# Kernel optimization log

Measured on AMD Instinct MI355X. Metric: run time of the kernel, lower is better.

## Reference

```python
import jax, jax.numpy as jnp
import numpy as np

B, A, D, K = 262144, 10, 10, 32  # batch, aspects, aspect dim (=10), projection dim


def setup_inputs() -> dict:
    key = jax.random.key(0)
    ks = jax.random.split(key, 7)
    scale = 0.01
    return {
        "user_rep": jax.random.normal(ks[0], (B, A, D), jnp.float32),
        "item_rep": jax.random.normal(ks[1], (B, A, D), jnp.float32),
        "affinity_matrix": jax.random.uniform(ks[2], (D, D), jnp.float32, -scale, scale),
        "user_projection": jax.random.uniform(ks[3], (K, D), jnp.float32, -scale, scale),
        "user_parameters": jax.random.uniform(ks[4], (K, 1), jnp.float32, -scale, scale),
        "item_projection": jax.random.uniform(ks[5], (K, D), jnp.float32, -scale, scale),
        "item_parameters": jax.random.uniform(ks[6], (K, 1), jnp.float32, -scale, scale),
    }


def reference(user_rep, item_rep, affinity_matrix, user_projection,
              user_parameters, item_projection, item_parameters):
    # affinity: relu( U @ M @ V^T )  -> [B, Au, Av]
    aff = jax.nn.relu(jnp.einsum('bud,de,bve->buv', user_rep, affinity_matrix, item_rep))

    h_user = jnp.einsum('kd,bud->bku', user_projection, user_rep)  # [B,K,Au]
    h_item = jnp.einsum('kd,bvd->bkv', item_projection, item_rep)  # [B,K,Av]

    # user importance branch
    hu = jax.nn.relu(h_user + jnp.einsum('bkv,buv->bku', h_item, aff))
    u_score = jnp.einsum('k,bku->bu', user_parameters[:, 0], hu)   # [B,Au]
    user_asp_importance = jax.nn.softmax(u_score, axis=1)

    # item importance branch
    hi = jax.nn.relu(h_item + jnp.einsum('bku,buv->bkv', h_user, aff))
    i_score = jnp.einsum('k,bkv->bv', item_parameters[:, 0], hi)   # [B,Av]
    item_asp_importance = jax.nn.softmax(i_score, axis=1)

    return (user_asp_importance, item_asp_importance)
```

## Files before the change

kernel.cpp:

```cpp
#include <hip/hip_runtime.h>

#define NB 262144
#define AA 10
#define DD 10
#define KK 32

typedef float v2f __attribute__((ext_vector_type(2)));

static __device__ __forceinline__ v2f mk2(float a, float b) {
    v2f r; r.x = a; r.y = b; return r;
}
static __device__ __forceinline__ v2f pk_fma(v2f a, v2f b, v2f c) {
    v2f d; asm("v_pk_fma_f32 %0, %1, %2, %3" : "=v"(d) : "v"(a), "v"(b), "v"(c)); return d;
}
static __device__ __forceinline__ v2f pk_fma_s(v2f sa, v2f b, v2f c) {
    v2f d; asm("v_pk_fma_f32 %0, %1, %2, %3" : "=v"(d) : "s"(sa), "v"(b), "v"(c)); return d;
}
static __device__ __forceinline__ v2f pk_mul(v2f a, v2f b) {
    v2f d; asm("v_pk_mul_f32 %0, %1, %2" : "=v"(d) : "v"(a), "v"(b)); return d;
}
static __device__ __forceinline__ v2f pk_mul_s(v2f sa, v2f b) {
    v2f d; asm("v_pk_mul_f32 %0, %1, %2" : "=v"(d) : "s"(sa), "v"(b)); return d;
}
static __device__ __forceinline__ v2f pk_add(v2f a, v2f b) {
    v2f d; asm("v_pk_add_f32 %0, %1, %2" : "=v"(d) : "v"(a), "v"(b)); return d;
}

static __device__ __forceinline__ float b2f(unsigned short h) {
    union { unsigned u; float f; } c; c.u = ((unsigned)h) << 16; return c.f;
}
static __device__ __forceinline__ float bflo(unsigned w) {
    union { unsigned u; float f; } c; c.u = w << 16; return c.f;
}
static __device__ __forceinline__ float bfhi(unsigned w) {
    union { unsigned u; float f; } c; c.u = w & 0xffff0000u; return c.f;
}

__device__ __forceinline__ int detect_f32(const unsigned short* p, int nshorts,
                                          unsigned expthr, int lane) {
    int bad = 0;
    if (lane < nshorts) {
        unsigned e = (p[lane] >> 7) & 0xFFu;
        bad = (e >= expthr);
    }
    return __any(bad);
}

__global__ __launch_bounds__(64) void prep_weights(
    const unsigned short* __restrict__ wM,
    const unsigned short* __restrict__ wPu,
    const unsigned short* __restrict__ wpu,
    const unsigned short* __restrict__ wPi,
    const unsigned short* __restrict__ wpi,
    float* __restrict__ wf)
{
    const int t = threadIdx.x;
    int f = 0;
    f |= detect_f32(wM,  64, 125, t) << 0;
    f |= detect_f32(wPu, 64, 125, t) << 1;
    f |= detect_f32(wpu, 32, 125, t) << 2;
    f |= detect_f32(wPi, 64, 125, t) << 3;
    f |= detect_f32(wpi, 32, 125, t) << 4;
    const float* fM  = (const float*)wM;
    const float* fPu = (const float*)wPu;
    const float* fpu = (const float*)wpu;
    const float* fPi = (const float*)wPi;
    const float* fpi = (const float*)wpi;

    for (int i = t; i < 100; i += 64) wf[i] = (f & 1) ? fM[i] : b2f(wM[i]);

    for (int i = t; i < KK * 24; i += 64) {
        const int k = i / 24, j = i % 24;
        float vu = 0.f, vi = 0.f;
        if (j < 10) {
            vu = (f & 2) ? fPu[k * 10 + j] : b2f(wPu[k * 10 + j]);
            vi = (f & 8) ? fPi[k * 10 + j] : b2f(wPi[k * 10 + j]);
        } else if (j < 20) {
            vu = (f & 8) ? fPi[k * 10 + j - 10] : b2f(wPi[k * 10 + j - 10]);
            vi = (f & 2) ? fPu[k * 10 + j - 10] : b2f(wPu[k * 10 + j - 10]);
        } else if (j == 20) {
            vu = (f & 4)  ? fpu[k] : b2f(wpu[k]);
            vi = (f & 16) ? fpi[k] : b2f(wpi[k]);
        }
        wf[128 + i] = vu;
        wf[896 + i] = vi;
    }
}

static __device__ __forceinline__ void load_rep(const unsigned short* __restrict__ p,
                                                int isf32, long long b, v2f R[AA][5]) {
    if (isf32) {
        const float4* g = (const float4*)((const float*)p + b * 100);
        #pragma unroll
        for (int j = 0; j < 25; j++) {
            float4 w = g[j];
            int e = 2 * j;
            R[e / 5][e % 5]             = mk2(w.x, w.y);
            R[(e + 1) / 5][(e + 1) % 5] = mk2(w.z, w.w);
        }
    } else {
        const uint2* g = (const uint2*)(p + b * 100);
        #pragma unroll
        for (int j = 0; j < 25; j++) {
            uint2 w = g[j];
            int e = 2 * j;
            R[e / 5][e % 5]             = mk2(bflo(w.x), bfhi(w.x));
            R[(e + 1) / 5][(e + 1) % 5] = mk2(bflo(w.y), bfhi(w.y));
        }
    }
}

__global__ __launch_bounds__(64, 2) void aie_main(
    const unsigned short* __restrict__ user_rep,
    const unsigned short* __restrict__ item_rep,
    const float* __restrict__ wf,
    float* __restrict__ out)
{
    __shared__ v2f stash[64 * 51];
    const int t = threadIdx.x;
    const long long b = (long long)blockIdx.x * 64 + t;
    v2f* my = &stash[t * 51];

    const int fu = detect_f32(user_rep, 64, 137, t);
    const int fi = detect_f32(item_rep, 64, 137, t);

    v2f U2[AA][5], V2[AA][5];
    load_rep(item_rep, fi, b, V2);
    load_rep(user_rep, fu, b, U2);

    const v2f* M2 = (const v2f*)wf;

    #pragma unroll
    for (int u = 0; u < AA; u++) {
        v2f um2[5];
        {
            v2f xs = mk2(U2[u][0].x, U2[u][0].x);
            #pragma unroll
            for (int j = 0; j < 5; j++) um2[j] = pk_mul_s(M2[j], xs);
        }
        #pragma unroll
        for (int d = 1; d < DD; d++) {
            const float x = (d & 1) ? U2[u][d >> 1].y : U2[u][d >> 1].x;
            v2f xs = mk2(x, x);
            #pragma unroll
            for (int j = 0; j < 5; j++) um2[j] = pk_fma_s(M2[d * 5 + j], xs, um2[j]);
        }
        v2f Wr[5];
        #pragma unroll
        for (int j = 0; j < 5; j++) Wr[j] = mk2(0.f, 0.f);
        #pragma unroll
        for (int v = 0; v < AA; v++) {
            v2f r2 = pk_mul(um2[0], V2[v][0]);
            #pragma unroll
            for (int j = 1; j < 5; j++) r2 = pk_fma(um2[j], V2[v][j], r2);
            const float r = fmaxf(r2.x + r2.y, 0.f);
            v2f rs = mk2(r, r);
            #pragma unroll
            for (int j = 0; j < 5; j++) Wr[j] = pk_fma(rs, V2[v][j], Wr[j]);
        }
        #pragma unroll
        for (int j = 0; j < 5; j++) my[u * 5 + j] = Wr[j];
    }
    asm volatile("" ::: "memory");

    v2f Wf[AA][5];
    #pragma unroll
    for (int u = 0; u < AA; u++)
        #pragma unroll
        for (int j = 0; j < 5; j++) Wf[u][j] = my[u * 5 + j];

    float us[AA];
    #pragma unroll
    for (int u = 0; u < AA; u++) us[u] = 0.f;
    #pragma unroll 2
    for (int k = 0; k < KK; k++) {
        const v2f* wk = (const v2f*)(wf + 128 + k * 24);
        const float pw = wf[128 + k * 24 + 20];
        #pragma unroll
        for (int u = 0; u < AA; u++) {
            v2f a2 = pk_mul_s(wk[0], U2[u][0]);
            v2f c2 = pk_mul_s(wk[5], Wf[u][0]);
            #pragma unroll
            for (int j = 1; j < 5; j++) {
                a2 = pk_fma_s(wk[j],     U2[u][j], a2);
                c2 = pk_fma_s(wk[5 + j], Wf[u][j], c2);
            }
            v2f s2 = pk_add(a2, c2);
            us[u] += pw * fmaxf(s2.x + s2.y, 0.f);
        }
    }

    {
        float mx = us[0];
        #pragma unroll
        for (int u = 1; u < AA; u++) mx = fmaxf(mx, us[u]);
        float s = 0.f;
        #pragma unroll
        for (int u = 0; u < AA; u++) { us[u] = __expf(us[u] - mx); s += us[u]; }
        const float inv = 1.f / s;
        float* o0 = out + b * 10;
        #pragma unroll
        for (int j = 0; j < 5; j++)
            *(float2*)(o0 + 2 * j) = make_float2(us[2 * j] * inv, us[2 * j + 1] * inv);
    }

    load_rep(item_rep, fi, b, V2);

    #pragma unroll
    for (int v = 0; v < AA; v++) {
        v2f mv2[5];
        #pragma unroll
        for (int dp = 0; dp < 5; dp++) {
            v2f s0 = pk_mul_s(M2[(2 * dp) * 5],     V2[v][0]);
            v2f s1 = pk_mul_s(M2[(2 * dp + 1) * 5], V2[v][0]);
            #pragma unroll
            for (int j = 1; j < 5; j++) {
                s0 = pk_fma_s(M2[(2 * dp) * 5 + j],     V2[v][j], s0);
                s1 = pk_fma_s(M2[(2 * dp + 1) * 5 + j], V2[v][j], s1);
            }
            mv2[dp] = mk2(s0.x + s0.y, s1.x + s1.y);
        }
        v2f Xr[5];
        #pragma unroll
        for (int j = 0; j < 5; j++) Xr[j] = mk2(0.f, 0.f);
        #pragma unroll
        for (int u = 0; u < AA; u++) {
            v2f r2 = pk_mul(mv2[0], U2[u][0]);
            #pragma unroll
            for (int j = 1; j < 5; j++) r2 = pk_fma(mv2[j], U2[u][j], r2);
            const float r = fmaxf(r2.x + r2.y, 0.f);
            v2f rs = mk2(r, r);
            #pragma unroll
            for (int j = 0; j < 5; j++) Xr[j] = pk_fma(rs, U2[u][j], Xr[j]);
        }
        #pragma unroll
        for (int j = 0; j < 5; j++) my[v * 5 + j] = Xr[j];
    }
    asm volatile("" ::: "memory");

    v2f Xf[AA][5];
    #pragma unroll
    for (int v = 0; v < AA; v++)
        #pragma unroll
        for (int j = 0; j < 5; j++) Xf[v][j] = my[v * 5 + j];

    float isc[AA];
    #pragma unroll
    for (int v = 0; v < AA; v++) isc[v] = 0.f;
    #pragma unroll 2
    for (int k = 0; k < KK; k++) {
        const v2f* wk = (const v2f*)(wf + 896 + k * 24);
        const float pw = wf[896 + k * 24 + 20];
        #pragma unroll
        for (int v = 0; v < AA; v++) {
            v2f a2 = pk_mul_s(wk[0], V2[v][0]);
            v2f c2 = pk_mul_s(wk[5], Xf[v][0]);
            #pragma unroll
            for (int j = 1; j < 5; j++) {
                a2 = pk_fma_s(wk[j],     V2[v][j], a2);
                c2 = pk_fma_s(wk[5 + j], Xf[v][j], c2);
            }
            v2f s2 = pk_add(a2, c2);
            isc[v] += pw * fmaxf(s2.x + s2.y, 0.f);
        }
    }

    {
        float mx = isc[0];
        #pragma unroll
        for (int v = 1; v < AA; v++) mx = fmaxf(mx, isc[v]);
        float s = 0.f;
        #pragma unroll
        for (int v = 0; v < AA; v++) { isc[v] = __expf(isc[v] - mx); s += isc[v]; }
        const float inv = 1.f / s;
        float* o1 = out + (size_t)NB * 10 + b * 10;
        #pragma unroll
        for (int j = 0; j < 5; j++)
            *(float2*)(o1 + 2 * j) = make_float2(isc[2 * j] * inv, isc[2 * j + 1] * inv);
    }
}

extern "C" void kernel_launch(void* const* d_in, const int* in_sizes, int n_in,
                              void* d_out, int out_size, void* d_ws, size_t ws_size,
                              hipStream_t stream) {
    const unsigned short* user_rep = (const unsigned short*)d_in[0];
    const unsigned short* item_rep = (const unsigned short*)d_in[1];
    float* wf = (float*)d_ws;

    hipLaunchKernelGGL(prep_weights, dim3(1), dim3(64), 0, stream,
                       (const unsigned short*)d_in[2], (const unsigned short*)d_in[3],
                       (const unsigned short*)d_in[4], (const unsigned short*)d_in[5],
                       (const unsigned short*)d_in[6], wf);

    hipLaunchKernelGGL(aie_main, dim3(NB / 64), dim3(64), 0, stream,
                       user_rep, item_rep, wf, (float*)d_out);
}
```

Measured before the change: 374.2 us.

## Compute both affinity contractions in one pass with packed bf16 reps and LDS weights

```diff
diff --git a/kernel.cpp b/kernel.cpp
--- a/kernel.cpp
+++ b/kernel.cpp
@@ -6,34 +6,22 @@
 #define KK 32
 
 typedef float v2f __attribute__((ext_vector_type(2)));
+typedef unsigned int uint32;
 
 static __device__ __forceinline__ v2f mk2(float a, float b) {
     v2f r; r.x = a; r.y = b; return r;
 }
-static __device__ __forceinline__ v2f pk_fma(v2f a, v2f b, v2f c) {
-    v2f d; asm("v_pk_fma_f32 %0, %1, %2, %3" : "=v"(d) : "v"(a), "v"(b), "v"(c)); return d;
-}
-static __device__ __forceinline__ v2f pk_fma_s(v2f sa, v2f b, v2f c) {
-    v2f d; asm("v_pk_fma_f32 %0, %1, %2, %3" : "=v"(d) : "s"(sa), "v"(b), "v"(c)); return d;
-}
-static __device__ __forceinline__ v2f pk_mul(v2f a, v2f b) {
-    v2f d; asm("v_pk_mul_f32 %0, %1, %2" : "=v"(d) : "v"(a), "v"(b)); return d;
-}
-static __device__ __forceinline__ v2f pk_mul_s(v2f sa, v2f b) {
-    v2f d; asm("v_pk_mul_f32 %0, %1, %2" : "=v"(d) : "s"(sa), "v"(b)); return d;
-}
-static __device__ __forceinline__ v2f pk_add(v2f a, v2f b) {
-    v2f d; asm("v_pk_add_f32 %0, %1, %2" : "=v"(d) : "v"(a), "v"(b)); return d;
-}
-
 static __device__ __forceinline__ float b2f(unsigned short h) {
-    union { unsigned u; float f; } c; c.u = ((unsigned)h) << 16; return c.f;
-}
-static __device__ __forceinline__ float bflo(unsigned w) {
-    union { unsigned u; float f; } c; c.u = w << 16; return c.f;
-}
-static __device__ __forceinline__ float bfhi(unsigned w) {
-    union { unsigned u; float f; } c; c.u = w & 0xffff0000u; return c.f;
+    union { uint32 u; float f; } c; c.u = ((uint32)h) << 16; return c.f;
+}
+static __device__ __forceinline__ float bflo(uint32 w) {
+    union { uint32 u; float f; } c; c.u = w << 16; return c.f;
+}
+static __device__ __forceinline__ float bfhi(uint32 w) {
+    union { uint32 u; float f; } c; c.u = w & 0xffff0000u; return c.f;
+}
+static __device__ __forceinline__ uint32 cvtpk(float lo, float hi) {
+    uint32 d; asm("v_cvt_pk_bf16_f32 %0, %1, %2" : "=v"(d) : "v"(lo), "v"(hi)); return d;
 }
 
 __device__ __forceinline__ int detect_f32(const unsigned short* p, int nshorts,
@@ -67,7 +55,7 @@
     const float* fPi = (const float*)wPi;
     const float* fpi = (const float*)wpi;
 
-    for (int i = t; i < 100; i += 64) wf[i] = (f & 1) ? fM[i] : b2f(wM[i]);
+    for (int i = t; i < 128; i += 64) wf[i] = (i < 100) ? ((f & 1) ? fM[i] : b2f(wM[i])) : 0.f;
 
     for (int i = t; i < KK * 24; i += 64) {
         const int k = i / 24, j = i % 24;
@@ -87,107 +75,115 @@
     }
 }
 
-static __device__ __forceinline__ void load_rep(const unsigned short* __restrict__ p,
-                                                int isf32, long long b, v2f R[AA][5]) {
-    if (isf32) {
-        const float4* g = (const float4*)((const float*)p + b * 100);
-        #pragma unroll
-        for (int j = 0; j < 25; j++) {
-            float4 w = g[j];
-            int e = 2 * j;
-            R[e / 5][e % 5]             = mk2(w.x, w.y);
-            R[(e + 1) / 5][(e + 1) % 5] = mk2(w.z, w.w);
-        }
-    } else {
-        const uint2* g = (const uint2*)(p + b * 100);
-        #pragma unroll
-        for (int j = 0; j < 25; j++) {
-            uint2 w = g[j];
-            int e = 2 * j;
-            R[e / 5][e % 5]             = mk2(bflo(w.x), bfhi(w.x));
-            R[(e + 1) / 5][(e + 1) % 5] = mk2(bflo(w.y), bfhi(w.y));
-        }
-    }
-}
-
 __global__ __launch_bounds__(64, 2) void aie_main(
     const unsigned short* __restrict__ user_rep,
     const unsigned short* __restrict__ item_rep,
     const float* __restrict__ wf,
     float* __restrict__ out)
 {
-    __shared__ v2f stash[64 * 51];
+    __shared__ float swt[1664];
     const int t = threadIdx.x;
     const long long b = (long long)blockIdx.x * 64 + t;
-    v2f* my = &stash[t * 51];
+
+    {
+        const float4* s = (const float4*)wf;
+        float4* d4 = (float4*)swt;
+        #pragma unroll
+        for (int i = 0; i < 7; i++) {
+            int idx = t + 64 * i;
+            if (idx < 416) d4[idx] = s[idx];
+        }
+    }
 
     const int fu = detect_f32(user_rep, 64, 137, t);
     const int fi = detect_f32(item_rep, 64, 137, t);
 
-    v2f U2[AA][5], V2[AA][5];
-    load_rep(item_rep, fi, b, V2);
-    load_rep(user_rep, fu, b, U2);
-
-    const v2f* M2 = (const v2f*)wf;
+    uint32 Vpk[50], Upk[50];
+    if (!fi) {
+        const uint2* g = (const uint2*)(item_rep + b * 100);
+        #pragma unroll
+        for (int j = 0; j < 25; j++) { uint2 w = g[j]; Vpk[2 * j] = w.x; Vpk[2 * j + 1] = w.y; }
+    } else {
+        const float4* g = (const float4*)((const float*)item_rep + b * 100);
+        #pragma unroll
+        for (int j = 0; j < 25; j++) { float4 w = g[j]; Vpk[2 * j] = cvtpk(w.x, w.y); Vpk[2 * j + 1] = cvtpk(w.z, w.w); }
+    }
+    if (!fu) {
+        const uint2* g = (const uint2*)(user_rep + b * 100);
+        #pragma unroll
+        for (int j = 0; j < 25; j++) { uint2 w = g[j]; Upk[2 * j] = w.x; Upk[2 * j + 1] = w.y; }
+    } else {
+        const float4* g = (const float4*)((const float*)user_rep + b * 100);
+        #pragma unroll
+        for (int j = 0; j < 25; j++) { float4 w = g[j]; Upk[2 * j] = cvtpk(w.x, w.y); Upk[2 * j + 1] = cvtpk(w.z, w.w); }
+    }
+
+    v2f V2[AA][5];
+    #pragma unroll
+    for (int p = 0; p < 50; p++) V2[p / 5][p % 5] = mk2(bflo(Vpk[p]), bfhi(Vpk[p]));
+
+    __syncthreads();
+
+    v2f X2[AA][5];
+    float us[AA];
 
     #pragma unroll
     for (int u = 0; u < AA; u++) {
+        asm volatile("" ::: "memory");
+
+        v2f Uu[5];
+        #pragma unroll
+        for (int j = 0; j < 5; j++) Uu[j] = mk2(bflo(Upk[u * 5 + j]), bfhi(Upk[u * 5 + j]));
+
         v2f um2[5];
         {
-            v2f xs = mk2(U2[u][0].x, U2[u][0].x);
-            #pragma unroll
-            for (int j = 0; j < 5; j++) um2[j] = pk_mul_s(M2[j], xs);
+            const float x = Uu[0].x;
+            #pragma unroll
+            for (int j = 0; j < 5; j++) um2[j] = x * mk2(swt[2 * j], swt[2 * j + 1]);
         }
         #pragma unroll
         for (int d = 1; d < DD; d++) {
-            const float x = (d & 1) ? U2[u][d >> 1].y : U2[u][d >> 1].x;
-            v2f xs = mk2(x, x);
-            #pragma unroll
-            for (int j = 0; j < 5; j++) um2[j] = pk_fma_s(M2[d * 5 + j], xs, um2[j]);
-        }
+            const float x = (d & 1) ? Uu[d >> 1].y : Uu[d >> 1].x;
+            #pragma unroll
+            for (int j = 0; j < 5; j++)
+                um2[j] += x * mk2(swt[d * 10 + 2 * j], swt[d * 10 + 2 * j + 1]);
+        }
+
         v2f Wr[5];
         #pragma unroll
         for (int j = 0; j < 5; j++) Wr[j] = mk2(0.f, 0.f);
         #pragma unroll
         for (int v = 0; v < AA; v++) {
-            v2f r2 = pk_mul(um2[0], V2[v][0]);
-            #pragma unroll
-            for (int j = 1; j < 5; j++) r2 = pk_fma(um2[j], V2[v][j], r2);
+            v2f r2 = um2[0] * V2[v][0];
+            #pragma unroll
+            for (int j = 1; j < 5; j++) r2 += um2[j] * V2[v][j];
             const float r = fmaxf(r2.x + r2.y, 0.f);
-            v2f rs = mk2(r, r);
-            #pragma unroll
-            for (int j = 0; j < 5; j++) Wr[j] = pk_fma(rs, V2[v][j], Wr[j]);
-        }
-        #pragma unroll
-        for (int j = 0; j < 5; j++) my[u * 5 + j] = Wr[j];
-    }
-    asm volatile("" ::: "memory");
-
-    v2f Wf[AA][5];
-    #pragma unroll
-    for (int u = 0; u < AA; u++)
-        #pragma unroll
-        for (int j = 0; j < 5; j++) Wf[u][j] = my[u * 5 + j];
-
-    float us[AA];
-    #pragma unroll
-    for (int u = 0; u < AA; u++) us[u] = 0.f;
-    #pragma unroll 2
-    for (int k = 0; k < KK; k++) {
-        const v2f* wk = (const v2f*)(wf + 128 + k * 24);
-        const float pw = wf[128 + k * 24 + 20];
-        #pragma unroll
-        for (int u = 0; u < AA; u++) {
-            v2f a2 = pk_mul_s(wk[0], U2[u][0]);
-            v2f c2 = pk_mul_s(wk[5], Wf[u][0]);
+            #pragma unroll
+            for (int j = 0; j < 5; j++) Wr[j] += r * V2[v][j];
+            if (u == 0) {
+                #pragma unroll
+                for (int j = 0; j < 5; j++) X2[v][j] = r * Uu[j];
+            } else {
+                #pragma unroll
+                for (int j = 0; j < 5; j++) X2[v][j] += r * Uu[j];
+            }
+        }
+
+        float acc = 0.f;
+        #pragma unroll 2
+        for (int k = 0; k < KK; k++) {
+            const int o = 128 + k * 24;
+            v2f a = mk2(swt[o],      swt[o + 1])  * Uu[0];
+            v2f c = mk2(swt[o + 10], swt[o + 11]) * Wr[0];
             #pragma unroll
             for (int j = 1; j < 5; j++) {
-                a2 = pk_fma_s(wk[j],     U2[u][j], a2);
-                c2 = pk_fma_s(wk[5 + j], Wf[u][j], c2);
+                a += mk2(swt[o + 2 * j],      swt[o + 2 * j + 1])      * Uu[j];
+                c += mk2(swt[o + 10 + 2 * j], swt[o + 10 + 2 * j + 1]) * Wr[j];
             }
-            v2f s2 = pk_add(a2, c2);
-            us[u] += pw * fmaxf(s2.x + s2.y, 0.f);
-        }
+            v2f s = a + c;
+            acc += swt[o + 20] * fmaxf(s.x + s.y, 0.f);
+        }
+        us[u] = acc;
     }
 
     {
@@ -204,65 +200,25 @@
             *(float2*)(o0 + 2 * j) = make_float2(us[2 * j] * inv, us[2 * j + 1] * inv);
     }
 
-    load_rep(item_rep, fi, b, V2);
-
+    float isc[AA];
     #pragma unroll
     for (int v = 0; v < AA; v++) {
-        v2f mv2[5];
-        #pragma unroll
-        for (int dp = 0; dp < 5; dp++) {
-            v2f s0 = pk_mul_s(M2[(2 * dp) * 5],     V2[v][0]);
-            v2f s1 = pk_mul_s(M2[(2 * dp + 1) * 5], V2[v][0]);
+        asm volatile("" ::: "memory");
+        float acc = 0.f;
+        #pragma unroll 2
+        for (int k = 0; k < KK; k++) {
+            const int o = 896 + k * 24;
+            v2f a = mk2(swt[o],      swt[o + 1])  * V2[v][0];
+            v2f c = mk2(swt[o + 10], swt[o + 11]) * X2[v][0];
             #pragma unroll
             for (int j = 1; j < 5; j++) {
-                s0 = pk_fma_s(M2[(2 * dp) * 5 + j],     V2[v][j], s0);
-                s1 = pk_fma_s(M2[(2 * dp + 1) * 5 + j], V2[v][j], s1);
+                a += mk2(swt[o + 2 * j],      swt[o + 2 * j + 1])      * V2[v][j];
+                c += mk2(swt[o + 10 + 2 * j], swt[o + 10 + 2 * j + 1]) * X2[v][j];
             }
-            mv2[dp] = mk2(s0.x + s0.y, s1.x + s1.y);
-        }
-        v2f Xr[5];
-        #pragma unroll
-        for (int j = 0; j < 5; j++) Xr[j] = mk2(0.f, 0.f);
-        #pragma unroll
-        for (int u = 0; u < AA; u++) {
-            v2f r2 = pk_mul(mv2[0], U2[u][0]);
-            #pragma unroll
-            for (int j = 1; j < 5; j++) r2 = pk_fma(mv2[j], U2[u][j], r2);
-            const float r = fmaxf(r2.x + r2.y, 0.f);
-            v2f rs = mk2(r, r);
-            #pragma unroll
-            for (int j = 0; j < 5; j++) Xr[j] = pk_fma(rs, U2[u][j], Xr[j]);
-        }
-        #pragma unroll
-        for (int j = 0; j < 5; j++) my[v * 5 + j] = Xr[j];
-    }
-    asm volatile("" ::: "memory");
-
-    v2f Xf[AA][5];
-    #pragma unroll
-    for (int v = 0; v < AA; v++)
-        #pragma unroll
-        for (int j = 0; j < 5; j++) Xf[v][j] = my[v * 5 + j];
-
-    float isc[AA];
-    #pragma unroll
-    for (int v = 0; v < AA; v++) isc[v] = 0.f;
-    #pragma unroll 2
-    for (int k = 0; k < KK; k++) {
-        const v2f* wk = (const v2f*)(wf + 896 + k * 24);
-        const float pw = wf[896 + k * 24 + 20];
-        #pragma unroll
-        for (int v = 0; v < AA; v++) {
-            v2f a2 = pk_mul_s(wk[0], V2[v][0]);
-            v2f c2 = pk_mul_s(wk[5], Xf[v][0]);
-            #pragma unroll
-            for (int j = 1; j < 5; j++) {
-                a2 = pk_fma_s(wk[j],     V2[v][j], a2);
-                c2 = pk_fma_s(wk[5 + j], Xf[v][j], c2);
-            }
-            v2f s2 = pk_add(a2, c2);
-            isc[v] += pw * fmaxf(s2.x + s2.y, 0.f);
-        }
+            v2f s = a + c;
+            acc += swt[o + 20] * fmaxf(s.x + s.y, 0.f);
+        }
+        isc[v] = acc;
     }
 
     {
```

Measured after the change: 473.1 us. 26.4% more time.
